# Performance work log

Measured on AMD Instinct MI355X. Metric: run time of the kernel, lower is better.

Reference implementation:

```python
import jax, jax.numpy as jnp
import numpy as np

WH, WW = 7, 7
DIM, HEADS = 256, 8


def make_table_index(wh, ww):
    # relative coords table (log-spaced CPB input) and relative position index
    ch = np.arange(-(wh - 1), wh, dtype=np.float32)
    cw = np.arange(-(ww - 1), ww, dtype=np.float32)
    t = np.stack(np.meshgrid(ch, cw, indexing='ij'), axis=-1)[None]  # [1,2wh-1,2ww-1,2]
    t = t.copy()
    t[..., 0] /= (wh - 1)
    t[..., 1] /= (ww - 1)
    t *= 8.0
    t = np.sign(t) * np.log2(np.abs(t) + 1.0) / np.log2(8.0)
    coords = np.stack(np.meshgrid(np.arange(wh), np.arange(ww), indexing='ij'))
    cf = coords.reshape(2, -1)
    rc = (cf[:, :, None] - cf[:, None, :]).transpose(1, 2, 0).copy()  # [N,N,2]
    rc[..., 0] += wh - 1
    rc[..., 1] += ww - 1
    rc[..., 0] *= 2 * ww - 1
    idx = rc.sum(-1)
    return t.astype(np.float32), idx.astype(np.int32)


def setup_inputs() -> dict:
    key = jax.random.key(0)
    ks = jax.random.split(key, 10)
    B_, N, C, H = 2048, WH * WW, DIM, HEADS
    table, idx = make_table_index(WH, WW)
    return {
        'x': jax.random.normal(ks[0], (B_, N, C), jnp.float32),
        'mask': jnp.zeros((64, N, N), jnp.float32),
        'qkv_w': jax.random.normal(ks[1], (3 * C, C), jnp.float32) * 0.02,
        'q_bias': jnp.zeros((C,), jnp.float32),
        'v_bias': jnp.zeros((C,), jnp.float32),
        'logit_scale': jnp.full((H, 1, 1), np.log(10.0), jnp.float32),
        'cpb_w1': jax.random.normal(ks[2], (512, 2), jnp.float32) * 0.02,
        'cpb_b1': jnp.zeros((512,), jnp.float32),
        'cpb_w2': jax.random.normal(ks[3], (H, 512), jnp.float32) * 0.02,
        'proj_w': jax.random.normal(ks[4], (C, C), jnp.float32) * 0.02,
        'proj_b': jnp.zeros((C,), jnp.float32),
        'rel_coords_table': jnp.asarray(table),
        'rel_pos_index': jnp.asarray(idx),
    }


def _l2norm(t):
    return t / jnp.maximum(jnp.linalg.norm(t, axis=-1, keepdims=True), 1e-12)


def reference(x, mask, qkv_w, q_bias, v_bias, logit_scale, cpb_w1, cpb_b1,
              cpb_w2, proj_w, proj_b, rel_coords_table, rel_pos_index):
    B_, N, C = x.shape
    H = logit_scale.shape[0]
    hd = C // H
    qkv_b = jnp.concatenate([q_bias, jnp.zeros_like(v_bias), v_bias])
    qkv = (x @ qkv_w.T + qkv_b).reshape(B_, N, 3, H, hd).transpose(2, 0, 3, 1, 4)
    q, k, v = qkv[0], qkv[1], qkv[2]  # [B_,H,N,hd]
    attn = jnp.einsum('bhnd,bhmd->bhnm', _l2norm(q), _l2norm(k))
    scale = jnp.exp(jnp.minimum(logit_scale, jnp.log(jnp.float32(100.0))))  # [H,1,1]
    attn = attn * scale[None]
    # CPB MLP -> relative position bias
    table = jax.nn.relu(rel_coords_table @ cpb_w1.T + cpb_b1) @ cpb_w2.T  # [1,Th,Tw,H]
    table = table.reshape(-1, H)
    bias = table[rel_pos_index.reshape(-1)].reshape(N, N, H).transpose(2, 0, 1)
    attn = attn + 16.0 * jax.nn.sigmoid(bias)[None]
    nW = mask.shape[0]
    attn = attn.reshape(B_ // nW, nW, H, N, N) + mask[None, :, None]
    attn = jax.nn.softmax(attn.reshape(B_, H, N, N), axis=-1)
    out = jnp.einsum('bhnm,bhmd->bhnd', attn, v).transpose(0, 2, 1, 3).reshape(B_, N, C)
    return out @ proj_w.T + proj_b
```

## Files before the change

kernel.cpp:

```cpp
#include <hip/hip_runtime.h>

#define DEV __device__ __forceinline__

typedef float  f32x4  __attribute__((ext_vector_type(4)));
typedef __bf16 bf16x8 __attribute__((ext_vector_type(8)));

DEV unsigned short f2bf(float f) {
  unsigned u = __float_as_uint(f);
  u += 0x7fffu + ((u >> 16) & 1u);
  return (unsigned short)(u >> 16);
}
DEV float bf2f(unsigned short v) { return __uint_as_float(((unsigned)v) << 16); }

DEV void cp16(const void* g, void* l) {
  __builtin_amdgcn_global_load_lds((const __attribute__((address_space(1))) void*)g,
                                   (__attribute__((address_space(3))) void*)l, 16, 0, 0);
}

__global__ __launch_bounds__(256) void prep_kernel(
    const float* __restrict__ qkv_w, const float* __restrict__ proj_w,
    const float* __restrict__ q_bias, const float* __restrict__ v_bias,
    unsigned short* __restrict__ wq, unsigned short* __restrict__ wp,
    float* __restrict__ qkvb)
{
  int gid = blockIdx.x * 256 + threadIdx.x;
  if (gid < 196608) wq[gid] = f2bf(qkv_w[gid]);
  else              wp[gid - 196608] = f2bf(proj_w[gid - 196608]);
  if (gid < 768)
    qkvb[gid] = (gid < 256) ? q_bias[gid] : ((gid < 512) ? 0.f : v_bias[gid - 512]);
}

__global__ __launch_bounds__(256) void xbf16(
    const float* __restrict__ X, unsigned short* __restrict__ Xb)
{
  size_t gid = (size_t)blockIdx.x * 256 + threadIdx.x;
  const float4* xp = (const float4*)X;
  float4 f0 = xp[2 * gid], f1 = xp[2 * gid + 1];
  uint4 u;
  u.x = f2bf(f0.x) | ((unsigned)f2bf(f0.y) << 16);
  u.y = f2bf(f0.z) | ((unsigned)f2bf(f0.w) << 16);
  u.z = f2bf(f1.x) | ((unsigned)f2bf(f1.y) << 16);
  u.w = f2bf(f1.z) | ((unsigned)f2bf(f1.w) << 16);
  ((uint4*)Xb)[gid] = u;
}

__global__ __launch_bounds__(64) void cpb_mlp(
    const float* __restrict__ tab, const float* __restrict__ w1,
    const float* __restrict__ b1, const float* __restrict__ w2,
    float* __restrict__ table16)
{
  int r = blockIdx.x;
  int t = threadIdx.x;
  float x0 = tab[r * 2 + 0], x1 = tab[r * 2 + 1];
  float part[8];
#pragma unroll
  for (int h = 0; h < 8; ++h) part[h] = 0.f;
  for (int j = t; j < 512; j += 64) {
    float hv = fmaxf(w1[j * 2 + 0] * x0 + w1[j * 2 + 1] * x1 + b1[j], 0.f);
#pragma unroll
    for (int h = 0; h < 8; ++h) part[h] += hv * w2[h * 512 + j];
  }
#pragma unroll
  for (int h = 0; h < 8; ++h) {
    float v = part[h];
    for (int off = 32; off > 0; off >>= 1) v += __shfl_down(v, off, 64);
    if (t == 0) table16[r * 8 + h] = 16.f / (1.f + expf(-v));
  }
}

__global__ __launch_bounds__(256) void bmb(
    const float* __restrict__ t16, const int* __restrict__ ridx,
    const float* __restrict__ mask, float* __restrict__ bias64,
    float* __restrict__ mask64)
{
  int gid = blockIdx.x * 256 + threadIdx.x;
  int p = gid & 4095, i = p >> 6, j = p & 63;
  bool valid = (i < 49) && (j < 49);
  if (gid < 32768) {
    int h = gid >> 12;
    bias64[gid] = valid ? t16[ridx[i * 49 + j] * 8 + h] : 0.f;
  } else {
    int g2 = gid - 32768;
    int w = g2 >> 12;
    mask64[g2] = valid ? mask[w * 2401 + i * 49 + j] : 0.f;
  }
}

__global__ __launch_bounds__(256) void gemm_qkv(
    const unsigned short* __restrict__ Xb, const unsigned short* __restrict__ W,
    const float* __restrict__ bias, unsigned short* __restrict__ qkv)
{
  __shared__ __align__(1024) unsigned short sA[128 * 64];
  __shared__ __align__(1024) unsigned short sB[128 * 64];
  const int t = threadIdx.x, w = t >> 6, l = t & 63, quad = l >> 4, l15 = l & 15;
  const int idx = blockIdx.x;
  const int x8 = idx & 7, local = idx >> 3;
  const int my = x8 * 98 + local / 6, bnb = local % 6;
  const int bm = my * 128, bn = bnb * 128;
  const int wm = (w >> 1) * 64, wn = (w & 1) * 64;
  const int srow = t >> 3, sch = t & 7;
  const int sc = sch ^ (srow & 7);

  const unsigned short* asrc = Xb + (size_t)(bm + srow) * 256 + sc * 8;
  const unsigned short* wsrc = W  + (size_t)(bn + srow) * 256 + sc * 8;

  f32x4 acc[4][4] = {};
  for (int kt = 0; kt < 4; ++kt) {
    const int k0 = kt << 6;
    if (kt) __syncthreads();
#pragma unroll
    for (int i = 0; i < 4; ++i) {
      cp16(asrc + (size_t)i * 32 * 256 + k0, sA + (i * 256 + w * 64) * 8);
      cp16(wsrc + (size_t)i * 32 * 256 + k0, sB + (i * 256 + w * 64) * 8);
    }
    __syncthreads();
#pragma unroll
    for (int kk = 0; kk < 2; ++kk) {
      bf16x8 xf[4], wf[4];
#pragma unroll
      for (int mt = 0; mt < 4; ++mt)
        xf[mt] = *(const bf16x8*)&sA[(wm + mt * 16 + l15) * 64 + (((4 * kk + quad) ^ (l15 & 7)) * 8)];
#pragma unroll
      for (int nt = 0; nt < 4; ++nt)
        wf[nt] = *(const bf16x8*)&sB[(wn + nt * 16 + l15) * 64 + (((4 * kk + quad) ^ (l15 & 7)) * 8)];
#pragma unroll
      for (int nt = 0; nt < 4; ++nt)
#pragma unroll
        for (int mt = 0; mt < 4; ++mt)
          acc[nt][mt] = __builtin_amdgcn_mfma_f32_16x16x32_bf16(wf[nt], xf[mt], acc[nt][mt], 0, 0, 0);
    }
  }
  const int nbase = bn + wn;
#pragma unroll
  for (int mA = 0; mA < 4; ++mA) {
    const int mrow = bm + wm + mA * 16 + l15;
    const unsigned bb = (unsigned)(((unsigned long long)mrow * 87652394ull) >> 32);
    const int tok = mrow - (int)bb * 49;
#pragma unroll
    for (int k = 0; k < 2; ++k) {
      const int n0 = nbase + k * 32;
      const int s = n0 >> 8, h = (n0 >> 5) & 7;
      const f32x4 b0 = *(const f32x4*)(bias + n0 + quad * 4);
      const f32x4 b1 = *(const f32x4*)(bias + n0 + 16 + quad * 4);
      const f32x4 a0 = acc[2 * k][mA], a1 = acc[2 * k + 1][mA];
      uint4 u;
      u.x = f2bf(a0[0] + b0[0]) | ((unsigned)f2bf(a0[1] + b0[1]) << 16);
      u.y = f2bf(a0[2] + b0[2]) | ((unsigned)f2bf(a0[3] + b0[3]) << 16);
      u.z = f2bf(a1[0] + b1[0]) | ((unsigned)f2bf(a1[1] + b1[1]) << 16);
      u.w = f2bf(a1[2] + b1[2]) | ((unsigned)f2bf(a1[3] + b1[3]) << 16);
      *(uint4*)(qkv + (size_t)((bb * 8u + h) * 3u + s) * 1568 + tok * 32 + quad * 8) = u;
    }
  }
}

__global__ __launch_bounds__(256) void attn2(
    const unsigned short* __restrict__ qkv, const float* __restrict__ logit_scale,
    const float* __restrict__ bias64, const float* __restrict__ mask64,
    unsigned short* __restrict__ aout)
{
  __shared__ __align__(1024) char smem[4 * 12544];
  const int w = threadIdx.x >> 6, l = threadIdx.x & 63, quad = l >> 4, l15 = l & 15;
  const int flat = blockIdx.x * 4 + w;
  const int b = flat >> 3, h = flat & 7;
  char* my = smem + w * 12544;
  unsigned short* vT = (unsigned short*)my;
  unsigned short* P  = (unsigned short*)(my + 4096);
  float* rk = (float*)(my + 12288);

  const unsigned short* qb = qkv + (size_t)flat * 4704;
  const unsigned short* kb = qb + 1568;
  const unsigned short* vb = qb + 3136;

  bf16x8 kf[4], qf[4];
#pragma unroll
  for (int mt = 0; mt < 4; ++mt) kf[mt] = *(const bf16x8*)(kb + (mt * 16 + l15) * 32 + quad * 8);
#pragma unroll
  for (int nt = 0; nt < 4; ++nt) qf[nt] = *(const bf16x8*)(qb + (nt * 16 + l15) * 32 + quad * 8);

  const float scale = __expf(fminf(logit_scale[h], 4.60517019f));
  float rqv[4];
#pragma unroll
  for (int nt = 0; nt < 4; ++nt) {
    float s = 0.f;
#pragma unroll
    for (int d = 0; d < 8; ++d) { float f = (float)qf[nt][d]; s += f * f; }
    s += __shfl_xor(s, 16, 64); s += __shfl_xor(s, 32, 64);
    rqv[nt] = scale / fmaxf(sqrtf(s), 1e-12f);
  }
#pragma unroll
  for (int mt = 0; mt < 4; ++mt) {
    float s = 0.f;
#pragma unroll
    for (int d = 0; d < 8; ++d) { float f = (float)kf[mt][d]; s += f * f; }
    s += __shfl_xor(s, 16, 64); s += __shfl_xor(s, 32, 64);
    if (quad == 0) rk[mt * 16 + l15] = 1.f / fmaxf(sqrtf(s), 1e-12f);
  }

  if (l < 49) {
    unsigned short vv[32];
#pragma unroll
    for (int c = 0; c < 4; ++c) *(uint4*)&vv[c * 8] = *(const uint4*)(vb + l * 32 + c * 8);
#pragma unroll
    for (int dp = 0; dp < 32; ++dp) {
      const int d = (((dp >> 2) & 1) << 4) + ((dp >> 3) << 2) + (dp & 3);
      vT[d * 64 + (((l >> 3) ^ (d & 7)) << 3) + (l & 7)] = vv[dp];
    }
  } else {
#pragma unroll
    for (int d = 0; d < 32; ++d)
      vT[d * 64 + (((l >> 3) ^ (d & 7)) << 3) + (l & 7)] = 0;
  }
  __syncthreads();

  f32x4 acc[4][4] = {};
#pragma unroll
  for (int mt = 0; mt < 4; ++mt)
#pragma unroll
    for (int nt = 0; nt < 4; ++nt)
      acc[mt][nt] = __builtin_amdgcn_mfma_f32_16x16x32_bf16(kf[mt], qf[nt], acc[mt][nt], 0, 0, 0);

  const float* bh = bias64 + (size_t)h * 4096;
  const float* mw = mask64 + (size_t)(b & 63) * 4096;
#pragma unroll
  for (int nt = 0; nt < 4; ++nt) {
    const int i = nt * 16 + l15;
    const float rqi = rqv[nt];
    float s[4][4];
    float mx = -1e30f;
#pragma unroll
    for (int mt = 0; mt < 4; ++mt) {
      const int jb = mt * 16 + quad * 4;
      const f32x4 b4  = *(const f32x4*)(bh + i * 64 + jb);
      const f32x4 m4  = *(const f32x4*)(mw + i * 64 + jb);
      const f32x4 rk4 = *(const f32x4*)(rk + jb);
#pragma unroll
      for (int r = 0; r < 4; ++r) {
        float sv = acc[mt][nt][r] * (rqi * rk4[r]) + b4[r] + m4[r];
        sv = (jb + r < 49) ? sv : -1e30f;
        s[mt][r] = sv;
        mx = fmaxf(mx, sv);
      }
    }
    mx = fmaxf(mx, __shfl_xor(mx, 16, 64));
    mx = fmaxf(mx, __shfl_xor(mx, 32, 64));
    float sum = 0.f;
    float p[4][4];
#pragma unroll
    for (int mt = 0; mt < 4; ++mt)
#pragma unroll
      for (int r = 0; r < 4; ++r) {
        float pv = __expf(s[mt][r] - mx);
        p[mt][r] = pv; sum += pv;
      }
    sum += __shfl_xor(sum, 16, 64);
    sum += __shfl_xor(sum, 32, 64);
    const float rs = 1.f / sum;
#pragma unroll
    for (int mt = 0; mt < 4; ++mt) {
      unsigned d0 = f2bf(p[mt][0] * rs) | ((unsigned)f2bf(p[mt][1] * rs) << 16);
      unsigned d1 = f2bf(p[mt][2] * rs) | ((unsigned)f2bf(p[mt][3] * rs) << 16);
      const int c = 2 * mt + (quad >> 1);
      uint2 uv; uv.x = d0; uv.y = d1;
      *(uint2*)((char*)P + i * 128 + ((c ^ (i & 7)) * 16) + (quad & 1) * 8) = uv;
    }
  }
  __syncthreads();

  f32x4 oacc[2][4] = {};
#pragma unroll
  for (int kk = 0; kk < 2; ++kk) {
    bf16x8 vf[2], pf[4];
#pragma unroll
    for (int mt = 0; mt < 2; ++mt)
      vf[mt] = *(const bf16x8*)((char*)vT + (mt * 16 + l15) * 128 + (((4 * kk + quad) ^ (l15 & 7)) * 16));
#pragma unroll
    for (int nt = 0; nt < 4; ++nt)
      pf[nt] = *(const bf16x8*)((char*)P + (nt * 16 + l15) * 128 + (((4 * kk + quad) ^ (l15 & 7)) * 16));
#pragma unroll
    for (int mt = 0; mt < 2; ++mt)
#pragma unroll
      for (int nt = 0; nt < 4; ++nt)
        oacc[mt][nt] = __builtin_amdgcn_mfma_f32_16x16x32_bf16(vf[mt], pf[nt], oacc[mt][nt], 0, 0, 0);
  }

#pragma unroll
  for (int nt = 0; nt < 4; ++nt) {
    const int tok = nt * 16 + l15;
    if (tok < 49) {
      unsigned short* op = aout + (size_t)(b * 49 + tok) * 256 + h * 32;
#pragma unroll
      for (int mt = 0; mt < 2; ++mt) {
        unsigned u0 = f2bf(oacc[mt][nt][0]) | ((unsigned)f2bf(oacc[mt][nt][1]) << 16);
        unsigned u1 = f2bf(oacc[mt][nt][2]) | ((unsigned)f2bf(oacc[mt][nt][3]) << 16);
        uint2 uv; uv.x = u0; uv.y = u1;
        *(uint2*)(op + mt * 16 + quad * 4) = uv;
      }
    }
  }
}

__global__ __launch_bounds__(256) void gemm_proj(
    const unsigned short* __restrict__ A, const unsigned short* __restrict__ W,
    const float* __restrict__ bias, float* __restrict__ Y)
{
  __shared__ __align__(1024) unsigned short sA[128 * 64];
  __shared__ __align__(1024) unsigned short sB[128 * 64];
  const int t = threadIdx.x, w = t >> 6, l = t & 63, quad = l >> 4, l15 = l & 15;
  const int bm = blockIdx.y * 128, bn = blockIdx.x * 128;
  const int wm = (w >> 1) * 64, wn = (w & 1) * 64;
  const int srow = t >> 3, sch = t & 7;
  const int sc = sch ^ (srow & 7);

  f32x4 acc[4][4] = {};
  for (int kt = 0; kt < 4; ++kt) {
    const int k0 = kt << 6;
    if (kt) __syncthreads();
#pragma unroll
    for (int i = 0; i < 4; ++i) {
      const int row = i * 32 + srow;
      cp16(A + (size_t)(bm + row) * 256 + k0 + sc * 8, sA + (i * 256 + w * 64) * 8);
      cp16(W + (size_t)(bn + row) * 256 + k0 + sc * 8, sB + (i * 256 + w * 64) * 8);
    }
    __syncthreads();
#pragma unroll
    for (int kk = 0; kk < 2; ++kk) {
      bf16x8 xf[4], wf[4];
#pragma unroll
      for (int mt = 0; mt < 4; ++mt)
        xf[mt] = *(const bf16x8*)&sA[(wm + mt * 16 + l15) * 64 + (((4 * kk + quad) ^ (l15 & 7)) * 8)];
#pragma unroll
      for (int nt = 0; nt < 4; ++nt)
        wf[nt] = *(const bf16x8*)&sB[(wn + nt * 16 + l15) * 64 + (((4 * kk + quad) ^ (l15 & 7)) * 8)];
#pragma unroll
      for (int nt = 0; nt < 4; ++nt)
#pragma unroll
        for (int mt = 0; mt < 4; ++mt)
          acc[nt][mt] = __builtin_amdgcn_mfma_f32_16x16x32_bf16(wf[nt], xf[mt], acc[nt][mt], 0, 0, 0);
    }
  }
#pragma unroll
  for (int mA = 0; mA < 4; ++mA) {
    const int row = bm + wm + mA * 16 + l15;
    float* orow = Y + (size_t)row * 256;
#pragma unroll
    for (int nW = 0; nW < 4; ++nW) {
      const int c0 = bn + wn + nW * 16 + quad * 4;
      const f32x4 bv = *(const f32x4*)(bias + c0);
      f32x4 v = acc[nW][mA];
      v[0] += bv[0]; v[1] += bv[1]; v[2] += bv[2]; v[3] += bv[3];
      *(f32x4*)(orow + c0) = v;
    }
  }
}

extern "C" void kernel_launch(void* const* d_in, const int* in_sizes, int n_in,
                              void* d_out, int out_size, void* d_ws, size_t ws_size,
                              hipStream_t stream) {
  const float* x           = (const float*)d_in[0];
  const float* mask        = (const float*)d_in[1];
  const float* qkv_w       = (const float*)d_in[2];
  const float* q_bias      = (const float*)d_in[3];
  const float* v_bias      = (const float*)d_in[4];
  const float* logit_scale = (const float*)d_in[5];
  const float* cpb_w1      = (const float*)d_in[6];
  const float* cpb_b1      = (const float*)d_in[7];
  const float* cpb_w2      = (const float*)d_in[8];
  const float* proj_w      = (const float*)d_in[9];
  const float* proj_b      = (const float*)d_in[10];
  const float* rel_tab     = (const float*)d_in[11];
  const int*   rel_idx     = (const int*)d_in[12];
  float*       out         = (float*)d_out;

  char* ws = (char*)d_ws;
  unsigned short* qkvp    = (unsigned short*)(ws + 0);
  unsigned short* aows    = (unsigned short*)(ws + 154140672);
  unsigned short* wq      = (unsigned short*)(ws + 205520896);
  unsigned short* wp      = (unsigned short*)(ws + 205914112);
  float*          qkvb    = (float*)(ws + 206045184);
  float*          table16 = (float*)(ws + 206048256);
  float*          bias64  = (float*)(ws + 206053888);
  float*          mask64  = (float*)(ws + 206184960);
  unsigned short* xbf = aows;

  prep_kernel<<<1024, 256, 0, stream>>>(qkv_w, proj_w, q_bias, v_bias, wq, wp, qkvb);
  cpb_mlp<<<169, 64, 0, stream>>>(rel_tab, cpb_w1, cpb_b1, cpb_w2, table16);
  bmb<<<1152, 256, 0, stream>>>(table16, rel_idx, mask, bias64, mask64);
  xbf16<<<12544, 256, 0, stream>>>(x, xbf);
  gemm_qkv<<<4704, 256, 0, stream>>>(xbf, wq, qkvb, qkvp);
  attn2<<<4096, 256, 0, stream>>>(qkvp, logit_scale, bias64, mask64, aows);
  gemm_proj<<<dim3(2, 784), 256, 0, stream>>>(aows, wp, proj_b, out);
}
```

Measured before the change: 389.8 us.

## Streamline attention kernel: drop block barriers, defer softmax normalization, native bf16 casts

Replaces the two __syncthreads in the attention kernel with per-wave lgkmcnt waits, since each wave works only on its own LDS region. Moves softmax normalization after the PV MFMA so the 1/sum scale is applied to the output. Folds the padding mask into the precomputed bias (-1e30 for pad columns), which removes a per-element select. Also hoists the rk loads, adds s_setprio around the MFMA blocks, and switches manual bf16 rounding to native __bf16 casts. The barrier removal depends on each wave only reading LDS it wrote itself, and the native cast may round differently from the manual routine.

```diff
diff --git a/kernel.cpp b/kernel.cpp
--- a/kernel.cpp
+++ b/kernel.cpp
@@ -3,6 +3,7 @@
 #define DEV __device__ __forceinline__
 
 typedef float  f32x4  __attribute__((ext_vector_type(4)));
+typedef __bf16 bf16x4 __attribute__((ext_vector_type(4)));
 typedef __bf16 bf16x8 __attribute__((ext_vector_type(8)));
 
 DEV unsigned short f2bf(float f) {
@@ -10,7 +11,6 @@
   u += 0x7fffu + ((u >> 16) & 1u);
   return (unsigned short)(u >> 16);
 }
-DEV float bf2f(unsigned short v) { return __uint_as_float(((unsigned)v) << 16); }
 
 DEV void cp16(const void* g, void* l) {
   __builtin_amdgcn_global_load_lds((const __attribute__((address_space(1))) void*)g,
@@ -36,12 +36,10 @@
   size_t gid = (size_t)blockIdx.x * 256 + threadIdx.x;
   const float4* xp = (const float4*)X;
   float4 f0 = xp[2 * gid], f1 = xp[2 * gid + 1];
-  uint4 u;
-  u.x = f2bf(f0.x) | ((unsigned)f2bf(f0.y) << 16);
-  u.y = f2bf(f0.z) | ((unsigned)f2bf(f0.w) << 16);
-  u.z = f2bf(f1.x) | ((unsigned)f2bf(f1.y) << 16);
-  u.w = f2bf(f1.z) | ((unsigned)f2bf(f1.w) << 16);
-  ((uint4*)Xb)[gid] = u;
+  bf16x8 u;
+  u[0] = (__bf16)f0.x; u[1] = (__bf16)f0.y; u[2] = (__bf16)f0.z; u[3] = (__bf16)f0.w;
+  u[4] = (__bf16)f1.x; u[5] = (__bf16)f1.y; u[6] = (__bf16)f1.z; u[7] = (__bf16)f1.w;
+  ((bf16x8*)Xb)[gid] = u;
 }
 
 __global__ __launch_bounds__(64) void cpb_mlp(
@@ -78,7 +76,7 @@
   bool valid = (i < 49) && (j < 49);
   if (gid < 32768) {
     int h = gid >> 12;
-    bias64[gid] = valid ? t16[ridx[i * 49 + j] * 8 + h] : 0.f;
+    bias64[gid] = valid ? t16[ridx[i * 49 + j] * 8 + h] : -1e30f;
   } else {
     int g2 = gid - 32768;
     int w = g2 >> 12;
@@ -143,12 +141,12 @@
       const f32x4 b0 = *(const f32x4*)(bias + n0 + quad * 4);
       const f32x4 b1 = *(const f32x4*)(bias + n0 + 16 + quad * 4);
       const f32x4 a0 = acc[2 * k][mA], a1 = acc[2 * k + 1][mA];
-      uint4 u;
-      u.x = f2bf(a0[0] + b0[0]) | ((unsigned)f2bf(a0[1] + b0[1]) << 16);
-      u.y = f2bf(a0[2] + b0[2]) | ((unsigned)f2bf(a0[3] + b0[3]) << 16);
-      u.z = f2bf(a1[0] + b1[0]) | ((unsigned)f2bf(a1[1] + b1[1]) << 16);
-      u.w = f2bf(a1[2] + b1[2]) | ((unsigned)f2bf(a1[3] + b1[3]) << 16);
-      *(uint4*)(qkv + (size_t)((bb * 8u + h) * 3u + s) * 1568 + tok * 32 + quad * 8) = u;
+      bf16x8 u;
+      u[0] = (__bf16)(a0[0] + b0[0]); u[1] = (__bf16)(a0[1] + b0[1]);
+      u[2] = (__bf16)(a0[2] + b0[2]); u[3] = (__bf16)(a0[3] + b0[3]);
+      u[4] = (__bf16)(a1[0] + b1[0]); u[5] = (__bf16)(a1[1] + b1[1]);
+      u[6] = (__bf16)(a1[2] + b1[2]); u[7] = (__bf16)(a1[3] + b1[3]);
+      *(bf16x8*)(qkv + (size_t)((bb * 8u + h) * 3u + s) * 1568 + tok * 32 + quad * 8) = u;
     }
   }
 }
@@ -210,17 +208,25 @@
     for (int d = 0; d < 32; ++d)
       vT[d * 64 + (((l >> 3) ^ (d & 7)) << 3) + (l & 7)] = 0;
   }
-  __syncthreads();
 
   f32x4 acc[4][4] = {};
+  __builtin_amdgcn_s_setprio(1);
 #pragma unroll
   for (int mt = 0; mt < 4; ++mt)
 #pragma unroll
     for (int nt = 0; nt < 4; ++nt)
       acc[mt][nt] = __builtin_amdgcn_mfma_f32_16x16x32_bf16(kf[mt], qf[nt], acc[mt][nt], 0, 0, 0);
+  __builtin_amdgcn_s_setprio(0);
+
+  asm volatile("s_waitcnt lgkmcnt(0)" ::: "memory");
 
   const float* bh = bias64 + (size_t)h * 4096;
   const float* mw = mask64 + (size_t)(b & 63) * 4096;
+  f32x4 rk4v[4];
+#pragma unroll
+  for (int mt = 0; mt < 4; ++mt) rk4v[mt] = *(const f32x4*)(rk + mt * 16 + quad * 4);
+
+  float rs4[4];
 #pragma unroll
   for (int nt = 0; nt < 4; ++nt) {
     const int i = nt * 16 + l15;
@@ -230,13 +236,11 @@
 #pragma unroll
     for (int mt = 0; mt < 4; ++mt) {
       const int jb = mt * 16 + quad * 4;
-      const f32x4 b4  = *(const f32x4*)(bh + i * 64 + jb);
-      const f32x4 m4  = *(const f32x4*)(mw + i * 64 + jb);
-      const f32x4 rk4 = *(const f32x4*)(rk + jb);
+      const f32x4 b4 = *(const f32x4*)(bh + i * 64 + jb);
+      const f32x4 m4 = *(const f32x4*)(mw + i * 64 + jb);
 #pragma unroll
       for (int r = 0; r < 4; ++r) {
-        float sv = acc[mt][nt][r] * (rqi * rk4[r]) + b4[r] + m4[r];
-        sv = (jb + r < 49) ? sv : -1e30f;
+        float sv = fmaf(acc[mt][nt][r], rqi * rk4v[mt][r], b4[r] + m4[r]);
         s[mt][r] = sv;
         mx = fmaxf(mx, sv);
       }
@@ -254,17 +258,18 @@
       }
     sum += __shfl_xor(sum, 16, 64);
     sum += __shfl_xor(sum, 32, 64);
-    const float rs = 1.f / sum;
+    rs4[nt] = 1.f / sum;
 #pragma unroll
     for (int mt = 0; mt < 4; ++mt) {
-      unsigned d0 = f2bf(p[mt][0] * rs) | ((unsigned)f2bf(p[mt][1] * rs) << 16);
-      unsigned d1 = f2bf(p[mt][2] * rs) | ((unsigned)f2bf(p[mt][3] * rs) << 16);
+      bf16x4 pk;
+      pk[0] = (__bf16)p[mt][0]; pk[1] = (__bf16)p[mt][1];
+      pk[2] = (__bf16)p[mt][2]; pk[3] = (__bf16)p[mt][3];
       const int c = 2 * mt + (quad >> 1);
-      uint2 uv; uv.x = d0; uv.y = d1;
-      *(uint2*)((char*)P + i * 128 + ((c ^ (i & 7)) * 16) + (quad & 1) * 8) = uv;
-    }
-  }
-  __syncthreads();
+      *(bf16x4*)((char*)P + i * 128 + ((c ^ (i & 7)) * 16) + (quad & 1) * 8) = pk;
+    }
+  }
+
+  asm volatile("s_waitcnt lgkmcnt(0)" ::: "memory");
 
   f32x4 oacc[2][4] = {};
 #pragma unroll
@@ -276,11 +281,13 @@
 #pragma unroll
     for (int nt = 0; nt < 4; ++nt)
       pf[nt] = *(const bf16x8*)((char*)P + (nt * 16 + l15) * 128 + (((4 * kk + quad) ^ (l15 & 7)) * 16));
+    __builtin_amdgcn_s_setprio(1);
 #pragma unroll
     for (int mt = 0; mt < 2; ++mt)
 #pragma unroll
       for (int nt = 0; nt < 4; ++nt)
         oacc[mt][nt] = __builtin_amdgcn_mfma_f32_16x16x32_bf16(vf[mt], pf[nt], oacc[mt][nt], 0, 0, 0);
+    __builtin_amdgcn_s_setprio(0);
   }
 
 #pragma unroll
@@ -288,12 +295,13 @@
     const int tok = nt * 16 + l15;
     if (tok < 49) {
       unsigned short* op = aout + (size_t)(b * 49 + tok) * 256 + h * 32;
+      const float rs = rs4[nt];
 #pragma unroll
       for (int mt = 0; mt < 2; ++mt) {
-        unsigned u0 = f2bf(oacc[mt][nt][0]) | ((unsigned)f2bf(oacc[mt][nt][1]) << 16);
-        unsigned u1 = f2bf(oacc[mt][nt][2]) | ((unsigned)f2bf(oacc[mt][nt][3]) << 16);
-        uint2 uv; uv.x = u0; uv.y = u1;
-        *(uint2*)(op + mt * 16 + quad * 4) = uv;
+        bf16x4 ov;
+        ov[0] = (__bf16)(oacc[mt][nt][0] * rs); ov[1] = (__bf16)(oacc[mt][nt][1] * rs);
+        ov[2] = (__bf16)(oacc[mt][nt][2] * rs); ov[3] = (__bf16)(oacc[mt][nt][3] * rs);
+        *(bf16x4*)(op + mt * 16 + quad * 4) = ov;
       }
     }
   }
```

Result: no change. 389.5 us (-0.1%).
